# Optimization experiments

Measured on AMD Instinct MI355X. Metric: run time of the kernel, lower is better.

Reference implementation:

```python
import jax, jax.numpy as jnp
import numpy as np

B, T = 2048, 512
H1, H2, H3 = 100, 60, 30


def _glorot(key, shape, fan):
    bound = 1.0 / np.sqrt(fan)
    return jax.random.uniform(key, shape, jnp.float32, -bound, bound)


def setup_inputs() -> dict:
    key = jax.random.key(0)
    ks = jax.random.split(key, 17)
    inp = {"x": jax.random.normal(ks[0], (B, T, 2), jnp.float32)}
    # layer 1: input 2 -> hidden 100
    inp["W_ih1"] = _glorot(ks[1], (H1, 2), H1)
    inp["W_hh1"] = _glorot(ks[2], (H1, H1), H1)
    inp["b_ih1"] = _glorot(ks[3], (H1,), H1)
    inp["b_hh1"] = _glorot(ks[4], (H1,), H1)
    # layer 2: 100 -> 60
    inp["W_ih2"] = _glorot(ks[5], (H2, H1), H2)
    inp["W_hh2"] = _glorot(ks[6], (H2, H2), H2)
    inp["b_ih2"] = _glorot(ks[7], (H2,), H2)
    inp["b_hh2"] = _glorot(ks[8], (H2,), H2)
    # layer 3: 60 -> 30
    inp["W_ih3"] = _glorot(ks[9], (H3, H2), H3)
    inp["W_hh3"] = _glorot(ks[10], (H3, H3), H3)
    inp["b_ih3"] = _glorot(ks[11], (H3,), H3)
    inp["b_hh3"] = _glorot(ks[12], (H3,), H3)
    # heads
    inp["W_o1"] = _glorot(ks[13], (10, H3), 10)
    inp["b_o1"] = _glorot(ks[14], (10,), 10)
    inp["W_o2"] = _glorot(ks[15], (2, 10), 2)
    inp["b_o2"] = _glorot(ks[16], (2,), 2)
    return inp


def rnn_layer(x, W_ih, W_hh, b_ih, b_hh):
    # x: [B, T, in]; precompute the time-parallel input projection once
    xp = jnp.einsum("bti,hi->bth", x, W_ih) + (b_ih + b_hh)  # [B, T, H]
    h0 = jnp.zeros((x.shape[0], W_hh.shape[0]), x.dtype)

    def step(h, xt):  # xt: [B, H]
        h = jnp.tanh(xt + h @ W_hh.T)
        return h, h

    _, ys = jax.lax.scan(step, h0, jnp.swapaxes(xp, 0, 1))  # [T, B, H]
    return jnp.swapaxes(ys, 0, 1)  # [B, T, H]


def reference(x, W_ih1, W_hh1, b_ih1, b_hh1, W_ih2, W_hh2, b_ih2, b_hh2,
              W_ih3, W_hh3, b_ih3, b_hh3, W_o1, b_o1, W_o2, b_o2):
    h = rnn_layer(x, W_ih1, W_hh1, b_ih1, b_hh1)
    h = rnn_layer(h, W_ih2, W_hh2, b_ih2, b_hh2)
    h = rnn_layer(h, W_ih3, W_hh3, b_ih3, b_hh3)
    o = jnp.einsum("bth,oh->bto", h, W_o1) + b_o1
    return jnp.einsum("bto,po->btp", o, W_o2) + b_o2  # [B, T, 2]
```

## Files before the change

### kernel.cpp

```cpp
#include <hip/hip_runtime.h>

typedef _Float16 v8hf __attribute__((ext_vector_type(8)));
typedef float    v4f  __attribute__((ext_vector_type(4)));

#define MFMA16(a, b, c) __builtin_amdgcn_mfma_f32_16x16x32_f16((a), (b), (c), 0, 0, 0)

#define TT 512
#define BT 16
#define NTH 512

#define PBLK  8192u
#define H2OFF 4352u
#define H3OFF 6656u
#define XSTO  16384u
#define RINGO 49152u

__shared__ __align__(64) char SM[57344];

__device__ __forceinline__ v4f tanh4(v4f r) {
    const float KS = 2.8853900817779268f;
    const float CL = 13.8498724f;
    float z0 = __builtin_amdgcn_fmed3f(r[0] * KS, -CL, CL);
    float z1 = __builtin_amdgcn_fmed3f(r[1] * KS, -CL, CL);
    float z2 = __builtin_amdgcn_fmed3f(r[2] * KS, -CL, CL);
    float z3 = __builtin_amdgcn_fmed3f(r[3] * KS, -CL, CL);
    float a0 = __builtin_amdgcn_exp2f(z0) + 1.f;
    float a1 = __builtin_amdgcn_exp2f(z1) + 1.f;
    float a2 = __builtin_amdgcn_exp2f(z2) + 1.f;
    float a3 = __builtin_amdgcn_exp2f(z3) + 1.f;
    float P = a0 * a1, Q = a2 * a3;
    float R = __builtin_amdgcn_rcpf(P * Q);
    float iP = Q * R, iQ = P * R;
    v4f t;
    t[0] = 1.f - 2.f * (a1 * iP);
    t[1] = 1.f - 2.f * (a0 * iP);
    t[2] = 1.f - 2.f * (a3 * iQ);
    t[3] = 1.f - 2.f * (a2 * iQ);
    return t;
}

__global__ __launch_bounds__(NTH)
void rnn3_sp(const float* __restrict__ xg,
             const float* __restrict__ Wih1, const float* __restrict__ Whh1,
             const float* __restrict__ bih1, const float* __restrict__ bhh1,
             const float* __restrict__ Wih2, const float* __restrict__ Whh2,
             const float* __restrict__ bih2, const float* __restrict__ bhh2,
             const float* __restrict__ Wih3, const float* __restrict__ Whh3,
             const float* __restrict__ bih3, const float* __restrict__ bhh3,
             const float* __restrict__ Wo1,  const float* __restrict__ bo1,
             const float* __restrict__ Wo2,  const float* __restrict__ bo2,
             float* __restrict__ outg)
{
    const int tid   = threadIdx.x;
    const int lane  = tid & 63;
    const int wid   = tid >> 6;
    const int col   = lane & 15;
    const int g     = lane >> 4;
    const int bbase = blockIdx.x * BT;

    {
        float4 z = {0.f, 0.f, 0.f, 0.f};
        float4* p4 = (float4*)SM;
        for (int i = tid; i < 1024; i += NTH) p4[i] = z;
        for (int i = tid; i < BT * TT * 2; i += NTH) {
            float v = xg[(size_t)bbase * (TT * 2) + i];
            int b = i >> 10, r = i & 1023, t = r >> 1, c = r & 1;
            *(_Float16*)(SM + XSTO + (unsigned)t * 64u + (unsigned)b * 4u + (unsigned)c * 2u) = (_Float16)v;
        }
    }

    v8hf F[14];
    #pragma unroll
    for (int i = 0; i < 14; ++i) F[i] = (v8hf)(_Float16)0.f;
    float bb0 = 0.f, bb1 = 0.f, bb2 = 0.f;

    auto ldW = [&](const float* W, int rows, int cols, int j, int kt) -> v8hf {
        v8hf r;
        #pragma unroll
        for (int e = 0; e < 8; ++e) {
            const int k = kt * 32 + g * 8 + e;
            float v = (j < rows && k < cols) ? W[j * cols + k] : 0.f;
            r[e] = (_Float16)v;
        }
        return r;
    };
    auto ldW1 = [&](int j, int kt) -> v8hf {
        v8hf r;
        #pragma unroll
        for (int e = 0; e < 8; ++e) {
            const int k = kt * 32 + g * 8 + e;
            float v = 0.f;
            if (j < 100) {
                if (k < 100)       v = Whh1[j * 100 + k];
                else if (k == 112) v = Wih1[j * 2];
                else if (k == 113) v = Wih1[j * 2 + 1];
            }
            r[e] = (_Float16)v;
        }
        return r;
    };
    auto bL1 = [&](int j) -> float { return (j < 100) ? bih1[j] + bhh1[j] : 0.f; };
    auto bL2 = [&](int j) -> float { return (j < 60) ? bih2[j] + bhh2[j] : 0.f; };
    auto bL3 = [&](int j) -> float { return (j < 30) ? bih3[j] + bhh3[j] : 0.f; };

    unsigned bRd = 0, bRd2 = 0, bRd3 = 0, bW1 = 0, bW2 = 0, bW3 = 0, bXw = 0, bRw = 0;
    unsigned xr = 0;

    if (wid < 4) {
        const int jA = 16 * wid + col;
        #pragma unroll
        for (int kt = 0; kt < 4; ++kt) {
            F[0 + kt] = ldW1(jA, kt);
            F[8 + kt] = ldW(Wih2, 60, 100, jA, kt);
        }
        F[12] = ldW(Whh2, 60, 60, jA, 0);
        F[13] = ldW(Whh2, 60, 60, jA, 1);
        bb0 = bL1(jA); bb2 = bL2(jA);
        if (wid < 3) {
            const int jB = jA + 64;
            #pragma unroll
            for (int kt = 0; kt < 4; ++kt) F[4 + kt] = ldW1(jB, kt);
            bb1 = bL1(jB);
        }
        bRd  = (unsigned)col * 272u + (unsigned)g * 16u;
        bRd2 = (unsigned)col * 144u + (unsigned)g * 16u;
        bW1  = (unsigned)(4 * g) * 272u + (unsigned)jA * 2u;
        bW2  = (unsigned)(4 * g) * 144u + (unsigned)jA * 2u;
    } else if (wid < 6) {
        const int j3 = 16 * (wid - 4) + col;
        F[0] = ldW(Wih3, 30, 60, j3, 0);
        F[1] = ldW(Wih3, 30, 60, j3, 1);
        F[2] = ldW(Whh3, 30, 30, j3, 0);
        bb0 = bL3(j3);
        bRd2 = (unsigned)col * 144u + (unsigned)g * 16u;
        bRd3 = (unsigned)col * 80u + (unsigned)g * 16u;
        bW3  = (unsigned)(4 * g) * 80u + (unsigned)j3 * 2u;
    } else if (wid == 6) {
        #pragma unroll
        for (int e = 0; e < 8; ++e) {
            const int k = g * 8 + e;
            float v = 0.f;
            if (col < 2 && k < 30) {
                #pragma unroll
                for (int u = 0; u < 10; ++u) v += Wo2[col * 10 + u] * Wo1[u * 30 + k];
            }
            F[0][e] = (_Float16)v;
        }
        if (col < 2) {
            float bv = bo2[col];
            #pragma unroll
            for (int u = 0; u < 10; ++u) bv += Wo2[col * 10 + u] * bo1[u];
            bb0 = bv;
        }
        bRd3 = (unsigned)col * 80u + (unsigned)g * 16u;
        bXw  = (unsigned)lane * 272u + 224u;
        xr   = XSTO + 64u + (unsigned)lane * 4u;
        bRw  = RINGO + (unsigned)(4 * g) * 512u + (unsigned)col * 4u;
    }

    __syncthreads();
    if (tid < BT)
        *(unsigned*)(SM + (unsigned)tid * 272u + 224u) =
            *(const unsigned*)(SM + XSTO + (unsigned)tid * 4u);
    __syncthreads();

    if (wid < 4) __builtin_amdgcn_s_setprio(1);

    auto flushfn = [&](int s) {
        const int tbase = s - 35;
        const unsigned rb = RINGO + (((unsigned)tbase & 63u) >> 1) * 16u;
        #pragma unroll
        for (int jj = 0; jj < 4; ++jj) {
            const int f = lane + 64 * jj;
            const int b = f >> 4, k = f & 15;
            float4 v = *(const float4*)(SM + rb + (unsigned)b * 512u + (unsigned)k * 16u);
            *(float4*)(outg + ((size_t)(bbase + b) * TT + tbase) * 2 + 4 * k) = v;
        }
    };

#define PHASE(RP, L1ON, L2ON, L3ON, HDON, XON, S) do {                                   \
    const unsigned RB_ = (RP) ? PBLK : 0u;                                               \
    const unsigned WB_ = (RP) ? 0u : PBLK;                                               \
    if (wid < 4) {                                                                       \
        if ((L1ON) || (L2ON)) {                                                          \
            v8hf A0 = *(const v8hf*)(SM + bRd + RB_ + 0u);                               \
            v8hf A1 = *(const v8hf*)(SM + bRd + RB_ + 64u);                              \
            v8hf A2 = *(const v8hf*)(SM + bRd + RB_ + 128u);                             \
            v8hf A3 = *(const v8hf*)(SM + bRd + RB_ + 192u);                             \
            if (L1ON) {                                                                  \
                { v4f p = {bb0, bb0, bb0, bb0}, q = {0.f, 0.f, 0.f, 0.f};                \
                  p = MFMA16(A0, F[0], p); q = MFMA16(A1, F[1], q);                      \
                  p = MFMA16(A2, F[2], p); q = MFMA16(A3, F[3], q);                      \
                  v4f r = tanh4(p + q);                                                  \
                  *(_Float16*)(SM + bW1 + WB_ + 0u)   = (_Float16)r[0];                  \
                  *(_Float16*)(SM + bW1 + WB_ + 272u) = (_Float16)r[1];                  \
                  *(_Float16*)(SM + bW1 + WB_ + 544u) = (_Float16)r[2];                  \
                  *(_Float16*)(SM + bW1 + WB_ + 816u) = (_Float16)r[3]; }                \
                if (wid < 3) {                                                           \
                  v4f p = {bb1, bb1, bb1, bb1}, q = {0.f, 0.f, 0.f, 0.f};                \
                  p = MFMA16(A0, F[4], p); q = MFMA16(A1, F[5], q);                      \
                  p = MFMA16(A2, F[6], p); q = MFMA16(A3, F[7], q);                      \
                  v4f r = tanh4(p + q);                                                  \
                  *(_Float16*)(SM + bW1 + WB_ + 128u)  = (_Float16)r[0];                 \
                  *(_Float16*)(SM + bW1 + WB_ + 400u)  = (_Float16)r[1];                 \
                  *(_Float16*)(SM + bW1 + WB_ + 672u)  = (_Float16)r[2];                 \
                  *(_Float16*)(SM + bW1 + WB_ + 944u)  = (_Float16)r[3]; }               \
            }                                                                            \
            if (L2ON) {                                                                  \
                v8hf B0 = *(const v8hf*)(SM + bRd2 + WB_ + H2OFF + 0u);                  \
                v8hf B1 = *(const v8hf*)(SM + bRd2 + WB_ + H2OFF + 64u);                 \
                v4f p = {bb2, bb2, bb2, bb2}, q = {0.f, 0.f, 0.f, 0.f};                  \
                p = MFMA16(A0, F[8],  p); q = MFMA16(A1, F[9],  q);                      \
                p = MFMA16(A2, F[10], p); q = MFMA16(A3, F[11], q);                      \
                p = MFMA16(B0, F[12], p); q = MFMA16(B1, F[13], q);                      \
                v4f r = tanh4(p + q);                                                    \
                *(_Float16*)(SM + bW2 + RB_ + H2OFF + 0u)   = (_Float16)r[0];            \
                *(_Float16*)(SM + bW2 + RB_ + H2OFF + 144u) = (_Float16)r[1];            \
                *(_Float16*)(SM + bW2 + RB_ + H2OFF + 288u) = (_Float16)r[2];            \
                *(_Float16*)(SM + bW2 + RB_ + H2OFF + 432u) = (_Float16)r[3];            \
            }                                                                            \
        }                                                                                \
    } else if (wid < 6) {                                                                \
        if (L3ON) {                                                                      \
            v8hf B0 = *(const v8hf*)(SM + bRd2 + WB_ + H2OFF + 0u);                      \
            v8hf B1 = *(const v8hf*)(SM + bRd2 + WB_ + H2OFF + 64u);                     \
            v8hf C0 = *(const v8hf*)(SM + bRd3 + RB_ + H3OFF);                           \
            v4f p = {bb0, bb0, bb0, bb0}, q = {0.f, 0.f, 0.f, 0.f};                      \
            p = MFMA16(B0, F[0], p); q = MFMA16(B1, F[1], q);                            \
            p = MFMA16(C0, F[2], p);                                                     \
            v4f r = tanh4(p + q);                                                        \
            *(_Float16*)(SM + bW3 + WB_ + H3OFF + 0u)   = (_Float16)r[0];                \
            *(_Float16*)(SM + bW3 + WB_ + H3OFF + 80u)  = (_Float16)r[1];                \
            *(_Float16*)(SM + bW3 + WB_ + H3OFF + 160u) = (_Float16)r[2];                \
            *(_Float16*)(SM + bW3 + WB_ + H3OFF + 240u) = (_Float16)r[3];                \
        }                                                                                \
    } else if (wid == 6) {                                                               \
        if (XON) {                                                                       \
            if (lane < 16) {                                                             \
                unsigned xv = *(const unsigned*)(SM + xr);                               \
                *(unsigned*)(SM + bXw + WB_) = xv;                                       \
            }                                                                            \
        }                                                                                \
        xr += 64u;                                                                       \
        if (HDON) {                                                                      \
            v8hf C0 = *(const v8hf*)(SM + bRd3 + RB_ + H3OFF);                           \
            v4f o = {bb0, bb0, bb0, bb0};                                                \
            o = MFMA16(C0, F[0], o);                                                     \
            const unsigned so = (((unsigned)(S) - 3u) & 63u) * 8u;                       \
            if (col < 2) {                                                               \
                *(float*)(SM + bRw + so + 0u)    = o[0];                                 \
                *(float*)(SM + bRw + so + 512u)  = o[1];                                 \
                *(float*)(SM + bRw + so + 1024u) = o[2];                                 \
                *(float*)(SM + bRw + so + 1536u) = o[3];                                 \
            }                                                                            \
        }                                                                                \
    } else {                                                                             \
        if ((S) >= 35 && (((S) - 4) & 31) == 31) flushfn((S));                           \
    }                                                                                    \
    __syncthreads();                                                                     \
} while (0)

    PHASE(0, 1, 0, 0, 0, 1, 0);
    PHASE(1, 1, 1, 0, 0, 1, 1);
    PHASE(0, 1, 1, 1, 0, 1, 2);
    PHASE(1, 1, 1, 1, 1, 1, 3);
    for (int s = 4; s < 510; s += 2) {
        PHASE(0, 1, 1, 1, 1, 1, s);
        PHASE(1, 1, 1, 1, 1, 1, s + 1);
    }
    PHASE(0, 1, 1, 1, 1, 1, 510);
    PHASE(1, 1, 1, 1, 1, 0, 511);
    PHASE(0, 0, 1, 1, 1, 0, 512);
    PHASE(1, 0, 0, 1, 1, 0, 513);
    PHASE(0, 0, 0, 0, 1, 0, 514);
    PHASE(1, 0, 0, 0, 0, 0, 515);
}

extern "C" void kernel_launch(void* const* d_in, const int* in_sizes, int n_in,
                              void* d_out, int out_size, void* d_ws, size_t ws_size,
                              hipStream_t stream) {
    (void)in_sizes; (void)n_in; (void)d_ws; (void)ws_size; (void)out_size;
    const float* x     = (const float*)d_in[0];
    const float* W_ih1 = (const float*)d_in[1];
    const float* W_hh1 = (const float*)d_in[2];
    const float* b_ih1 = (const float*)d_in[3];
    const float* b_hh1 = (const float*)d_in[4];
    const float* W_ih2 = (const float*)d_in[5];
    const float* W_hh2 = (const float*)d_in[6];
    const float* b_ih2 = (const float*)d_in[7];
    const float* b_hh2 = (const float*)d_in[8];
    const float* W_ih3 = (const float*)d_in[9];
    const float* W_hh3 = (const float*)d_in[10];
    const float* b_ih3 = (const float*)d_in[11];
    const float* b_hh3 = (const float*)d_in[12];
    const float* W_o1  = (const float*)d_in[13];
    const float* b_o1  = (const float*)d_in[14];
    const float* W_o2  = (const float*)d_in[15];
    const float* b_o2  = (const float*)d_in[16];
    float* out = (float*)d_out;

    rnn3_sp<<<2048 / BT, NTH, 0, stream>>>(
        x, W_ih1, W_hh1, b_ih1, b_hh1,
        W_ih2, W_hh2, b_ih2, b_hh2,
        W_ih3, W_hh3, b_ih3, b_hh3,
        W_o1, b_o1, W_o2, b_o2, out);
}
```

Measured before the change: 307.5 us.

## Spread RNN layer work across 16 waves, one 16-row tile per wave

Doubles the block to 1024 threads and gives each wave a single 16-row output tile: seven waves for layer 1, four for layer 2, two for layer 3, plus dedicated waves for x staging, the head, and output flushing. Before, four waves each computed two layer-1 tiles and a layer-2 tile back to back. The aim is to shorten the serial per-timestep critical path by running those matmuls in parallel, and to cut per-wave register use. In exchange, every phase barrier now synchronizes 16 waves instead of 8, and the layer-1 priority hint is dropped.

```diff
diff --git a/kernel.cpp b/kernel.cpp
--- a/kernel.cpp
+++ b/kernel.cpp
@@ -7,7 +7,7 @@
 
 #define TT 512
 #define BT 16
-#define NTH 512
+#define NTH 1024
 
 #define PBLK  8192u
 #define H2OFF 4352u
@@ -40,16 +40,16 @@
 }
 
 __global__ __launch_bounds__(NTH)
-void rnn3_sp(const float* __restrict__ xg,
-             const float* __restrict__ Wih1, const float* __restrict__ Whh1,
-             const float* __restrict__ bih1, const float* __restrict__ bhh1,
-             const float* __restrict__ Wih2, const float* __restrict__ Whh2,
-             const float* __restrict__ bih2, const float* __restrict__ bhh2,
-             const float* __restrict__ Wih3, const float* __restrict__ Whh3,
-             const float* __restrict__ bih3, const float* __restrict__ bhh3,
-             const float* __restrict__ Wo1,  const float* __restrict__ bo1,
-             const float* __restrict__ Wo2,  const float* __restrict__ bo2,
-             float* __restrict__ outg)
+void rnn3_t16(const float* __restrict__ xg,
+              const float* __restrict__ Wih1, const float* __restrict__ Whh1,
+              const float* __restrict__ bih1, const float* __restrict__ bhh1,
+              const float* __restrict__ Wih2, const float* __restrict__ Whh2,
+              const float* __restrict__ bih2, const float* __restrict__ bhh2,
+              const float* __restrict__ Wih3, const float* __restrict__ Whh3,
+              const float* __restrict__ bih3, const float* __restrict__ bhh3,
+              const float* __restrict__ Wo1,  const float* __restrict__ bo1,
+              const float* __restrict__ Wo2,  const float* __restrict__ bo2,
+              float* __restrict__ outg)
 {
     const int tid   = threadIdx.x;
     const int lane  = tid & 63;
@@ -69,10 +69,10 @@
         }
     }
 
-    v8hf F[14];
+    v8hf F[6];
     #pragma unroll
-    for (int i = 0; i < 14; ++i) F[i] = (v8hf)(_Float16)0.f;
-    float bb0 = 0.f, bb1 = 0.f, bb2 = 0.f;
+    for (int i = 0; i < 6; ++i) F[i] = (v8hf)(_Float16)0.f;
+    float bb0 = 0.f;
 
     auto ldW = [&](const float* W, int rows, int cols, int j, int kt) -> v8hf {
         v8hf r;
@@ -99,43 +99,40 @@
         }
         return r;
     };
-    auto bL1 = [&](int j) -> float { return (j < 100) ? bih1[j] + bhh1[j] : 0.f; };
-    auto bL2 = [&](int j) -> float { return (j < 60) ? bih2[j] + bhh2[j] : 0.f; };
-    auto bL3 = [&](int j) -> float { return (j < 30) ? bih3[j] + bhh3[j] : 0.f; };
 
     unsigned bRd = 0, bRd2 = 0, bRd3 = 0, bW1 = 0, bW2 = 0, bW3 = 0, bXw = 0, bRw = 0;
     unsigned xr = 0;
 
-    if (wid < 4) {
+    if (wid < 7) {
         const int jA = 16 * wid + col;
         #pragma unroll
-        for (int kt = 0; kt < 4; ++kt) {
-            F[0 + kt] = ldW1(jA, kt);
-            F[8 + kt] = ldW(Wih2, 60, 100, jA, kt);
-        }
-        F[12] = ldW(Whh2, 60, 60, jA, 0);
-        F[13] = ldW(Whh2, 60, 60, jA, 1);
-        bb0 = bL1(jA); bb2 = bL2(jA);
-        if (wid < 3) {
-            const int jB = jA + 64;
-            #pragma unroll
-            for (int kt = 0; kt < 4; ++kt) F[4 + kt] = ldW1(jB, kt);
-            bb1 = bL1(jB);
-        }
+        for (int kt = 0; kt < 4; ++kt) F[kt] = ldW1(jA, kt);
+        bb0 = (jA < 100) ? bih1[jA] + bhh1[jA] : 0.f;
+        bRd = (unsigned)col * 272u + (unsigned)g * 16u;
+        bW1 = (unsigned)(4 * g) * 272u + (unsigned)jA * 2u;
+    } else if (wid == 7) {
+        bXw = (unsigned)lane * 272u + 224u;
+        xr  = XSTO + 64u + (unsigned)lane * 4u;
+    } else if (wid < 12) {
+        const int j2 = 16 * (wid - 8) + col;
+        #pragma unroll
+        for (int kt = 0; kt < 4; ++kt) F[kt] = ldW(Wih2, 60, 100, j2, kt);
+        F[4] = ldW(Whh2, 60, 60, j2, 0);
+        F[5] = ldW(Whh2, 60, 60, j2, 1);
+        bb0 = (j2 < 60) ? bih2[j2] + bhh2[j2] : 0.f;
         bRd  = (unsigned)col * 272u + (unsigned)g * 16u;
         bRd2 = (unsigned)col * 144u + (unsigned)g * 16u;
-        bW1  = (unsigned)(4 * g) * 272u + (unsigned)jA * 2u;
-        bW2  = (unsigned)(4 * g) * 144u + (unsigned)jA * 2u;
-    } else if (wid < 6) {
-        const int j3 = 16 * (wid - 4) + col;
+        bW2  = (unsigned)(4 * g) * 144u + (unsigned)j2 * 2u;
+    } else if (wid < 14) {
+        const int j3 = 16 * (wid - 12) + col;
         F[0] = ldW(Wih3, 30, 60, j3, 0);
         F[1] = ldW(Wih3, 30, 60, j3, 1);
         F[2] = ldW(Whh3, 30, 30, j3, 0);
-        bb0 = bL3(j3);
+        bb0 = (j3 < 30) ? bih3[j3] + bhh3[j3] : 0.f;
         bRd2 = (unsigned)col * 144u + (unsigned)g * 16u;
         bRd3 = (unsigned)col * 80u + (unsigned)g * 16u;
         bW3  = (unsigned)(4 * g) * 80u + (unsigned)j3 * 2u;
-    } else if (wid == 6) {
+    } else if (wid == 14) {
         #pragma unroll
         for (int e = 0; e < 8; ++e) {
             const int k = g * 8 + e;
@@ -153,8 +150,6 @@
             bb0 = bv;
         }
         bRd3 = (unsigned)col * 80u + (unsigned)g * 16u;
-        bXw  = (unsigned)lane * 272u + 224u;
-        xr   = XSTO + 64u + (unsigned)lane * 4u;
         bRw  = RINGO + (unsigned)(4 * g) * 512u + (unsigned)col * 4u;
     }
 
@@ -164,8 +159,6 @@
             *(const unsigned*)(SM + XSTO + (unsigned)tid * 4u);
     __syncthreads();
 
-    if (wid < 4) __builtin_amdgcn_s_setprio(1);
-
     auto flushfn = [&](int s) {
         const int tbase = s - 35;
         const unsigned rb = RINGO + (((unsigned)tbase & 63u) >> 1) * 16u;
@@ -181,46 +174,48 @@
 #define PHASE(RP, L1ON, L2ON, L3ON, HDON, XON, S) do {                                   \
     const unsigned RB_ = (RP) ? PBLK : 0u;                                               \
     const unsigned WB_ = (RP) ? 0u : PBLK;                                               \
-    if (wid < 4) {                                                                       \
-        if ((L1ON) || (L2ON)) {                                                          \
+    if (wid < 7) {                                                                       \
+        if (L1ON) {                                                                      \
             v8hf A0 = *(const v8hf*)(SM + bRd + RB_ + 0u);                               \
             v8hf A1 = *(const v8hf*)(SM + bRd + RB_ + 64u);                              \
             v8hf A2 = *(const v8hf*)(SM + bRd + RB_ + 128u);                             \
             v8hf A3 = *(const v8hf*)(SM + bRd + RB_ + 192u);                             \
-            if (L1ON) {                                                                  \
-                { v4f p = {bb0, bb0, bb0, bb0}, q = {0.f, 0.f, 0.f, 0.f};                \
-                  p = MFMA16(A0, F[0], p); q = MFMA16(A1, F[1], q);                      \
-                  p = MFMA16(A2, F[2], p); q = MFMA16(A3, F[3], q);                      \
-                  v4f r = tanh4(p + q);                                                  \
-                  *(_Float16*)(SM + bW1 + WB_ + 0u)   = (_Float16)r[0];                  \
-                  *(_Float16*)(SM + bW1 + WB_ + 272u) = (_Float16)r[1];                  \
-                  *(_Float16*)(SM + bW1 + WB_ + 544u) = (_Float16)r[2];                  \
-                  *(_Float16*)(SM + bW1 + WB_ + 816u) = (_Float16)r[3]; }                \
-                if (wid < 3) {                                                           \
-                  v4f p = {bb1, bb1, bb1, bb1}, q = {0.f, 0.f, 0.f, 0.f};                \
-                  p = MFMA16(A0, F[4], p); q = MFMA16(A1, F[5], q);                      \
-                  p = MFMA16(A2, F[6], p); q = MFMA16(A3, F[7], q);                      \
-                  v4f r = tanh4(p + q);                                                  \
-                  *(_Float16*)(SM + bW1 + WB_ + 128u)  = (_Float16)r[0];                 \
-                  *(_Float16*)(SM + bW1 + WB_ + 400u)  = (_Float16)r[1];                 \
-                  *(_Float16*)(SM + bW1 + WB_ + 672u)  = (_Float16)r[2];                 \
-                  *(_Float16*)(SM + bW1 + WB_ + 944u)  = (_Float16)r[3]; }               \
+            v4f p = {bb0, bb0, bb0, bb0}, q = {0.f, 0.f, 0.f, 0.f};                      \
+            p = MFMA16(A0, F[0], p); q = MFMA16(A1, F[1], q);                            \
+            p = MFMA16(A2, F[2], p); q = MFMA16(A3, F[3], q);                            \
+            v4f r = tanh4(p + q);                                                        \
+            *(_Float16*)(SM + bW1 + WB_ + 0u)   = (_Float16)r[0];                        \
+            *(_Float16*)(SM + bW1 + WB_ + 272u) = (_Float16)r[1];                        \
+            *(_Float16*)(SM + bW1 + WB_ + 544u) = (_Float16)r[2];                        \
+            *(_Float16*)(SM + bW1 + WB_ + 816u) = (_Float16)r[3];                        \
+        }                                                                                \
+    } else if (wid == 7) {                                                               \
+        if (XON) {                                                                       \
+            if (lane < 16) {                                                             \
+                unsigned xv = *(const unsigned*)(SM + xr);                               \
+                *(unsigned*)(SM + bXw + WB_) = xv;                                       \
             }                                                                            \
-            if (L2ON) {                                                                  \
-                v8hf B0 = *(const v8hf*)(SM + bRd2 + WB_ + H2OFF + 0u);                  \
-                v8hf B1 = *(const v8hf*)(SM + bRd2 + WB_ + H2OFF + 64u);                 \
-                v4f p = {bb2, bb2, bb2, bb2}, q = {0.f, 0.f, 0.f, 0.f};                  \
-                p = MFMA16(A0, F[8],  p); q = MFMA16(A1, F[9],  q);                      \
-                p = MFMA16(A2, F[10], p); q = MFMA16(A3, F[11], q);                      \
-                p = MFMA16(B0, F[12], p); q = MFMA16(B1, F[13], q);                      \
-                v4f r = tanh4(p + q);                                                    \
-                *(_Float16*)(SM + bW2 + RB_ + H2OFF + 0u)   = (_Float16)r[0];            \
-                *(_Float16*)(SM + bW2 + RB_ + H2OFF + 144u) = (_Float16)r[1];            \
-                *(_Float16*)(SM + bW2 + RB_ + H2OFF + 288u) = (_Float16)r[2];            \
-                *(_Float16*)(SM + bW2 + RB_ + H2OFF + 432u) = (_Float16)r[3];            \
-            }                                                                            \
-        }                                                                                \
-    } else if (wid < 6) {                                                                \
+        }                                                                                \
+        xr += 64u;                                                                       \
+    } else if (wid < 12) {                                                               \
+        if (L2ON) {                                                                      \
+            v8hf A0 = *(const v8hf*)(SM + bRd + RB_ + 0u);                               \
+            v8hf A1 = *(const v8hf*)(SM + bRd + RB_ + 64u);                              \
+            v8hf A2 = *(const v8hf*)(SM + bRd + RB_ + 128u);                             \
+            v8hf A3 = *(const v8hf*)(SM + bRd + RB_ + 192u);                             \
+            v8hf B0 = *(const v8hf*)(SM + bRd2 + WB_ + H2OFF + 0u);                      \
+            v8hf B1 = *(const v8hf*)(SM + bRd2 + WB_ + H2OFF + 64u);                     \
+            v4f p = {bb0, bb0, bb0, bb0}, q = {0.f, 0.f, 0.f, 0.f};                      \
+            p = MFMA16(A0, F[0], p); q = MFMA16(A1, F[1], q);                            \
+            p = MFMA16(A2, F[2], p); q = MFMA16(A3, F[3], q);                            \
+            p = MFMA16(B0, F[4], p); q = MFMA16(B1, F[5], q);                            \
+            v4f r = tanh4(p + q);                                                        \
+            *(_Float16*)(SM + bW2 + RB_ + H2OFF + 0u)   = (_Float16)r[0];                \
+            *(_Float16*)(SM + bW2 + RB_ + H2OFF + 144u) = (_Float16)r[1];                \
+            *(_Float16*)(SM + bW2 + RB_ + H2OFF + 288u) = (_Float16)r[2];                \
+            *(_Float16*)(SM + bW2 + RB_ + H2OFF + 432u) = (_Float16)r[3];                \
+        }                                                                                \
+    } else if (wid < 14) {                                                               \
         if (L3ON) {                                                                      \
             v8hf B0 = *(const v8hf*)(SM + bRd2 + WB_ + H2OFF + 0u);                      \
             v8hf B1 = *(const v8hf*)(SM + bRd2 + WB_ + H2OFF + 64u);                     \
@@ -234,14 +229,7 @@
             *(_Float16*)(SM + bW3 + WB_ + H3OFF + 160u) = (_Float16)r[2];                \
             *(_Float16*)(SM + bW3 + WB_ + H3OFF + 240u) = (_Float16)r[3];                \
         }                                                                                \
-    } else if (wid == 6) {                                                               \
-        if (XON) {                                                                       \
-            if (lane < 16) {                                                             \
-                unsigned xv = *(const unsigned*)(SM + xr);                               \
-                *(unsigned*)(SM + bXw + WB_) = xv;                                       \
-            }                                                                            \
-        }                                                                                \
-        xr += 64u;                                                                       \
+    } else if (wid == 14) {                                                              \
         if (HDON) {                                                                      \
             v8hf C0 = *(const v8hf*)(SM + bRd3 + RB_ + H3OFF);                           \
             v4f o = {bb0, bb0, bb0, bb0};                                                \
@@ -299,7 +287,7 @@
     const float* b_o2  = (const float*)d_in[16];
     float* out = (float*)d_out;
 
-    rnn3_sp<<<2048 / BT, NTH, 0, stream>>>(
+    rnn3_t16<<<2048 / BT, NTH, 0, stream>>>(
         x, W_ih1, W_hh1, b_ih1, b_hh1,
         W_ih2, W_hh2, b_ih2, b_hh2,
         W_ih3, W_hh3, b_ih3, b_hh3,
```

New measurement: 291.8 us. 1.05x faster.
